# Optimization experiments

Measured on AMD Instinct MI355X. Metric: run time of the kernel, lower is better.

Reference implementation:

```python
import jax, jax.numpy as jnp
import numpy as np

EPS = 1e-5  # nn.LayerNorm default

def _ln(x, g, b):
    m = x.mean(-1, keepdims=True)
    v = ((x - m) ** 2).mean(-1, keepdims=True)
    return (x - m) / jnp.sqrt(v + EPS) * g + b


def setup_inputs() -> dict:
    key = jax.random.key(0)
    ks = jax.random.split(key, 16)
    B, T, H, W = 8, 20, 224, 224
    D, NC = 1536, 7
    s = 0.02
    f32 = jnp.float32
    return {
        'x': jax.random.normal(ks[0], (B, 3, T, H, W), f32),
        'timestamp': jax.random.uniform(ks[1], (B,), f32),
        # surrogate backbone: patchify conv (stride 16) + global avg pool -> 1536 feats
        'conv_w': jax.random.normal(ks[2], (D, 3, 16, 16), f32) * s,
        'conv_b': jnp.zeros((D,), f32),
        'w_red': jax.random.normal(ks[3], (D, D), f32) * s,
        'b_red': jnp.zeros((D,), f32),
        'w_num': jax.random.normal(ks[4], (D, 1), f32) * s,
        'b_num': jnp.zeros((D,), f32),
        'time_embed': jax.random.normal(ks[5], (1, T, D), f32) * s,
        'cls_swap': jax.random.normal(ks[6], (1, 5, 1, D), f32) * s,
        'ln_g': jnp.ones((D,), f32),
        'ln_b': jnp.zeros((D,), f32),
        'w_qkv': jax.random.normal(ks[7], (3 * D, D), f32) * s,
        'w_tproj': jax.random.normal(ks[8], (D, D), f32) * s,
        'b_tproj': jnp.zeros((D,), f32),
        'w_tfc': jax.random.normal(ks[9], (D, D), f32) * s,
        'b_tfc': jnp.zeros((D,), f32),
        'w_head': jax.random.normal(ks[10], (NC, D), f32) * s,
        'b_head': jnp.zeros((NC,), f32),
    }


def reference(x, timestamp, conv_w, conv_b, w_red, b_red, w_num, b_num,
              time_embed, cls_swap, ln_g, ln_b, w_qkv, w_tproj, b_tproj,
              w_tfc, b_tfc, w_head, b_head):
    B, C, T, H, W = x.shape
    D = w_red.shape[0]
    NH = 12
    HD = D // NH
    scale = HD ** -0.5

    # (b t) c h w  -> backbone surrogate -> (B*T, D)
    xf = jnp.transpose(x, (0, 2, 1, 3, 4)).reshape(B * T, C, H, W)
    f = jax.lax.conv_general_dilated(
        xf, conv_w, window_strides=(16, 16), padding='VALID',
        dimension_numbers=('NCHW', 'OIHW', 'NCHW'))
    f = (f + conv_b[None, :, None, None]).mean((2, 3))  # global avg pool -> (BT, D)

    xr = (f @ w_red.T + b_red).reshape(B, T, D)           # reduce_dim
    xt = xr + time_embed
    te = timestamp[:, None] @ w_num.T + b_num             # NumberToVector (B, D)
    xt = xt + te[:, None, :]

    # groups: b (n k) c -> b n k c, k=4, n=5; prepend 1 cls token per group
    g = jnp.concatenate(
        [jnp.broadcast_to(cls_swap, (B, 5, 1, D)), xt.reshape(B, 5, 4, D)], axis=2)

    for _ in range(4):  # num_interactions
        gr = g.reshape(B * 5, 5, D)
        hn = _ln(gr, ln_g, ln_b)
        qkv = (hn @ w_qkv.T).reshape(B * 5, 5, 3, NH, HD).transpose(2, 0, 3, 1, 4)
        q, k, v = qkv[0], qkv[1], qkv[2]                  # (b*n, h, t, hd)
        a = jax.nn.softmax(jnp.einsum('bhqd,bhkd->bhqk', q, k) * scale, axis=-1)
        o = jnp.einsum('bhqk,bhkd->bhqd', a, v).transpose(0, 2, 1, 3).reshape(B * 5, 5, D)
        o = o @ w_tproj.T + b_tproj                       # attn proj
        upd = (o @ w_tfc.T + b_tfc) + gr                  # temporal_fc + residual
        g = upd.reshape(B, 5, 5, D)
        # swap cls tokens between groups via roll
        g = g.at[:, :, 0, :].set(jnp.roll(g[:, :, 0, :], 1, axis=1))

    xt = g[:, :, 1:, :].reshape(B, T, D)
    out = xt[:, -1, :] + xr[:, -1, :]
    return out @ w_head.T + b_head  # (B, num_classes)
```

## Files before the change

kernel.cpp:

```cpp
#include <hip/hip_runtime.h>

typedef __attribute__((ext_vector_type(8))) short short8;
typedef __attribute__((ext_vector_type(8))) unsigned short ushort8;
typedef __attribute__((ext_vector_type(4))) float f32x4;
typedef unsigned short ushort_t;

__device__ __forceinline__ ushort_t f2bf(float f) {
    unsigned u = __builtin_bit_cast(unsigned, f);
    u += 0x7fffu + ((u >> 16) & 1u);
    return (ushort_t)(u >> 16);
}

__device__ __forceinline__ void load_lds16b(const void* gp, void* lp) {
    __builtin_amdgcn_global_load_lds(
        (const __attribute__((address_space(1))) void*)gp,
        (__attribute__((address_space(3))) void*)lp, 16, 0, 0);
}

__global__ __launch_bounds__(256, 2) void prep_kernel(
    const float* __restrict__ x, const float* __restrict__ w_qkv,
    const float* __restrict__ w_tf, const float* __restrict__ w_red,
    const float* __restrict__ conv_w, const float* __restrict__ w_tp,
    const float* __restrict__ b_tp, const float* __restrict__ b_tf,
    const float* __restrict__ conv_b, const float* __restrict__ b_red,
    const float* __restrict__ cls,
    ushort_t* __restrict__ AP, ushort_t* __restrict__ WQ,
    ushort_t* __restrict__ WF, ushort_t* __restrict__ WR,
    ushort_t* __restrict__ WCVT, ushort_t* __restrict__ WTT,
    float* __restrict__ BC, float* __restrict__ BC2,
    float* __restrict__ GA) {
    __shared__ __align__(16) float smem[64 * 68];
    int blk = blockIdx.x, tid = threadIdx.x;
    if (blk < 480) {
        int bt = blk / 3, c = blk % 3;
        int b = bt / 20, t = bt % 20;
        int w = tid >> 6, lane = tid & 63;
        int cl = lane < 56 ? lane : 55;
        const float* base = x + (size_t)((b * 3 + c) * 20 + t) * 50176
                              + (size_t)w * 224 + 4 * cl;
        f32x4 acc4[4];
        #pragma unroll
        for (int q = 0; q < 4; ++q) acc4[q] = (f32x4){0.f, 0.f, 0.f, 0.f};
        #pragma unroll
        for (int b16 = 0; b16 < 4; ++b16) {
            const int cnt = (b16 == 3) ? 8 : 16;
            f32x4 v[16];
            #pragma unroll
            for (int u = 0; u < 16; ++u) {
                if (u < cnt) {
                    int j = b16 * 16 + u;
                    v[u] = *(const f32x4*)(base + (size_t)j * 896);
                }
            }
            #pragma unroll
            for (int u = 0; u < 16; ++u)
                if (u < cnt) acc4[u & 3] += v[u];
        }
        if (lane >= 56) {
            #pragma unroll
            for (int q = 0; q < 4; ++q) acc4[q] = (f32x4){0.f, 0.f, 0.f, 0.f};
        }
        #pragma unroll
        for (int q = 0; q < 4; ++q) {
            #pragma unroll
            for (int m = 4; m <= 32; m <<= 1) {
                acc4[q][0] += __shfl_xor(acc4[q][0], m);
                acc4[q][1] += __shfl_xor(acc4[q][1], m);
                acc4[q][2] += __shfl_xor(acc4[q][2], m);
                acc4[q][3] += __shfl_xor(acc4[q][3], m);
            }
        }
        if (lane < 4) {
            #pragma unroll
            for (int q = 0; q < 4; ++q) {
                int i = w + 4 * q;
                ushort4 o;
                o.x = f2bf(acc4[q][0] * (1.f / 196.f));
                o.y = f2bf(acc4[q][1] * (1.f / 196.f));
                o.z = f2bf(acc4[q][2] * (1.f / 196.f));
                o.w = f2bf(acc4[q][3] * (1.f / 196.f));
                *(ushort4*)(AP + (size_t)bt * 768 + c * 256 + i * 16 + 4 * lane) = o;
            }
        }
    } else if (blk < 1920) {
        f32x4 va[4], vb[4];
        ushort_t* dst[4];
        long off[4];
        #pragma unroll
        for (int it = 0; it < 4; ++it) {
            long c = ((long)(blk - 480) * 4 + it) * 2048 + tid * 8;
            const float* s; ushort_t* d; long i;
            if (c < 7077888)       { s = w_qkv; d = WQ; i = c; }
            else if (c < 9437184)  { s = w_tf;  d = WF; i = c - 7077888; }
            else                   { s = w_red; d = WR; i = c - 9437184; }
            va[it] = *(const f32x4*)(s + i);
            vb[it] = *(const f32x4*)(s + i + 4);
            dst[it] = d; off[it] = i;
        }
        #pragma unroll
        for (int it = 0; it < 4; ++it) {
            ushort8 o;
            o[0] = f2bf(va[it][0]); o[1] = f2bf(va[it][1]);
            o[2] = f2bf(va[it][2]); o[3] = f2bf(va[it][3]);
            o[4] = f2bf(vb[it][0]); o[5] = f2bf(vb[it][1]);
            o[6] = f2bf(vb[it][2]); o[7] = f2bf(vb[it][3]);
            *(ushort8*)(dst[it] + off[it]) = o;
        }
    } else if (blk < 2496) {
        int tb = blk - 1920;
        int bi = tb / 24, bj = tb % 24;
        int r0 = (tid >> 4) << 2;
        int c0 = (tid & 15) << 2;
        #pragma unroll
        for (int rr = 0; rr < 4; ++rr) {
            f32x4 v = *(const f32x4*)(w_tp + (size_t)(bi * 64 + r0 + rr) * 1536 + bj * 64 + c0);
            smem[(r0 + rr) * 68 + c0 + 0] = v[0];
            smem[(r0 + rr) * 68 + c0 + 1] = v[1];
            smem[(r0 + rr) * 68 + c0 + 2] = v[2];
            smem[(r0 + rr) * 68 + c0 + 3] = v[3];
        }
        __syncthreads();
        #pragma unroll
        for (int rr = 0; rr < 4; ++rr) {
            int jj = r0 + rr;
            ushort4 o;
            o.x = f2bf(smem[(c0 + 0) * 68 + jj]);
            o.y = f2bf(smem[(c0 + 1) * 68 + jj]);
            o.z = f2bf(smem[(c0 + 2) * 68 + jj]);
            o.w = f2bf(smem[(c0 + 3) * 68 + jj]);
            *(ushort4*)(WTT + (size_t)(bj * 64 + jj) * 1536 + bi * 64 + c0) = o;
        }
    } else if (blk < 2784) {
        int tb = blk - 2496;
        int bi = tb / 12, bj = tb % 12;
        int r0 = (tid >> 4) << 2;
        int c0 = (tid & 15) << 2;
        #pragma unroll
        for (int rr = 0; rr < 4; ++rr) {
            f32x4 v = *(const f32x4*)(conv_w + (size_t)(bi * 64 + r0 + rr) * 768 + bj * 64 + c0);
            smem[(r0 + rr) * 68 + c0 + 0] = v[0];
            smem[(r0 + rr) * 68 + c0 + 1] = v[1];
            smem[(r0 + rr) * 68 + c0 + 2] = v[2];
            smem[(r0 + rr) * 68 + c0 + 3] = v[3];
        }
        __syncthreads();
        #pragma unroll
        for (int rr = 0; rr < 4; ++rr) {
            int jj = r0 + rr;
            ushort4 o;
            o.x = f2bf(smem[(c0 + 0) * 68 + jj]);
            o.y = f2bf(smem[(c0 + 1) * 68 + jj]);
            o.z = f2bf(smem[(c0 + 2) * 68 + jj]);
            o.w = f2bf(smem[(c0 + 3) * 68 + jj]);
            *(ushort4*)(WCVT + (size_t)(bj * 64 + jj) * 1536 + bi * 64 + c0) = o;
        }
    } else if (blk < 2824) {
        int cblk = blk - 2784;
        int b = cblk / 5, n = cblk % 5;
        size_t row = (size_t)(b * 25 + n * 5) * 1536;
        #pragma unroll
        for (int j = 0; j < 6; ++j) {
            int d = tid + j * 256;
            GA[row + d] = cls[n * 1536 + d];
        }
    } else if (blk < 2920) {
        int bb = blk - 2824;
        int row = bb * 16 + (tid >> 4);
        int sub = tid & 15;
        float acc = 0.f;
        for (int j = 0; j < 96; ++j) {
            int k = sub + j * 16;
            acc += w_tf[(size_t)row * 1536 + k] * b_tp[k];
        }
        acc += __shfl_xor(acc, 1); acc += __shfl_xor(acc, 2);
        acc += __shfl_xor(acc, 4); acc += __shfl_xor(acc, 8);
        if (sub == 0) BC[row] = acc + b_tf[row];
    } else {
        int bb = blk - 2920;
        int row = bb * 16 + (tid >> 4);
        int sub = tid & 15;
        float acc = 0.f;
        for (int j = 0; j < 48; ++j) {
            int n0 = sub + j * 16;
            acc += w_red[(size_t)row * 1536 + n0] * conv_b[n0];
            acc += w_red[(size_t)row * 1536 + n0 + 768] * conv_b[n0 + 768];
        }
        acc += __shfl_xor(acc, 1); acc += __shfl_xor(acc, 2);
        acc += __shfl_xor(acc, 4); acc += __shfl_xor(acc, 8);
        if (sub == 0) BC2[row] = acc + b_red[row];
    }
}

template <bool OUT_BF16>
__device__ __forceinline__ void gemm128_tile(
    char* lds, const ushort_t* __restrict__ A, const ushort_t* __restrict__ B,
    void* __restrict__ Cv, int M, int N, int K, int KS, int tn, int tm) {
    const int tid = threadIdx.x;
    const int lane = tid & 63;
    const int w = tid >> 6;
    const int wr = w >> 1, wc = w & 1;

    f32x4 acc[4][4];
    #pragma unroll
    for (int m = 0; m < 4; ++m)
        #pragma unroll
        for (int n = 0; n < 4; ++n)
            acc[m][n] = (f32x4){0.f, 0.f, 0.f, 0.f};

    const int nK = K >> 6;
    const int rbase = lane >> 3, cc = lane & 7;

    auto stage = [&](int k0, int buf) {
        char* lA = lds + buf * 32768;
        char* lB = lA + 16384;
        #pragma unroll
        for (int j = 0; j < 4; ++j) {
            int row = w * 32 + j * 8 + rbase;
            int cf = cc ^ (row & 7);
            int ga = tm * 128 + row; if (ga > M - 1) ga = M - 1;
            load_lds16b(A + (size_t)ga * KS + (k0 + cf * 8),
                        lA + (w * 32 + j * 8) * 128);
        }
        #pragma unroll
        for (int j = 0; j < 4; ++j) {
            int row = w * 32 + j * 8 + rbase;
            int cf = cc ^ (row & 7);
            load_lds16b(B + (size_t)(tn * 128 + row) * KS + (k0 + cf * 8),
                        lB + (w * 32 + j * 8) * 128);
        }
    };

    stage(0, 0);
    asm volatile("s_waitcnt vmcnt(0)" ::: "memory");
    __builtin_amdgcn_s_barrier();
    __builtin_amdgcn_sched_barrier(0);
    for (int t = 0; t < nK; ++t) {
        int cur = t & 1;
        if (t + 1 < nK) stage((t + 1) << 6, cur ^ 1);
        __builtin_amdgcn_sched_barrier(0);
        const char* lA = lds + cur * 32768;
        const char* lB = lA + 16384;
        #pragma unroll
        for (int ks = 0; ks < 2; ++ks) {
            short8 av[4], bv[4];
            const int rlo = lane & 15;
            const int chi = ks * 4 + (lane >> 4);
            #pragma unroll
            for (int m = 0; m < 4; ++m) {
                int r = wr * 64 + m * 16 + rlo;
                av[m] = *(const short8*)(lA + r * 128 + ((chi ^ (r & 7)) << 4));
            }
            #pragma unroll
            for (int n = 0; n < 4; ++n) {
                int r = wc * 64 + n * 16 + rlo;
                bv[n] = *(const short8*)(lB + r * 128 + ((chi ^ (r & 7)) << 4));
            }
            #pragma unroll
            for (int m = 0; m < 4; ++m)
                #pragma unroll
                for (int n = 0; n < 4; ++n)
                    acc[m][n] = __builtin_amdgcn_mfma_f32_16x16x32_bf16(
                        av[m], bv[n], acc[m][n], 0, 0, 0);
        }
        asm volatile("s_waitcnt vmcnt(0)" ::: "memory");
        __builtin_amdgcn_s_barrier();
        __builtin_amdgcn_sched_barrier(0);
    }

    const int c_l = lane & 15, r_q = (lane >> 4) * 4;
    #pragma unroll
    for (int m = 0; m < 4; ++m) {
        #pragma unroll
        for (int reg = 0; reg < 4; ++reg) {
            int r_ = tm * 128 + wr * 64 + m * 16 + r_q + reg;
            if (r_ < M) {
                #pragma unroll
                for (int n = 0; n < 4; ++n) {
                    int cc_ = tn * 128 + wc * 64 + n * 16 + c_l;
                    float v = acc[m][n][reg];
                    if (OUT_BF16) ((ushort_t*)Cv)[(size_t)r_ * N + cc_] = f2bf(v);
                    else          ((float*)Cv)[(size_t)r_ * N + cc_] = v;
                }
            }
        }
    }
}

__global__ __launch_bounds__(256) void wcf_kernel(
    const ushort_t* __restrict__ WF, const ushort_t* __restrict__ WTT,
    const ushort_t* __restrict__ WR, const ushort_t* __restrict__ WCVT,
    ushort_t* __restrict__ WC, ushort_t* __restrict__ WRC) {
    __shared__ __align__(16) char lds[65536];
    int task = blockIdx.x;
    if (task < 144)
        gemm128_tile<true>(lds, WF, WTT, WC, 1536, 1536, 1536, 1536,
                           task % 12, task / 12);
    else {
        int t2 = task - 144;
        gemm128_tile<true>(lds, WR, WCVT, WRC, 1536, 768, 1536, 1536,
                           t2 % 6, t2 / 6);
    }
}

template <int MT, bool OUT_BF16, bool HAS_BIAS, bool HAS_RES, bool CLS_SWAP, bool BUILD_G>
__device__ __forceinline__ void gemm_tile(
    char* lds, int lane, int tn, int tm,
    const ushort_t* __restrict__ A, const ushort_t* __restrict__ B,
    void* __restrict__ Cv, const float* __restrict__ bias,
    const float* __restrict__ res, int M, int N, int K, int KS,
    float* __restrict__ g_out, const float* __restrict__ temb,
    const float* __restrict__ ts, const float* __restrict__ w_num,
    const float* __restrict__ b_num) {
    constexpr int BUFB = MT * 2048 + 8192;

    f32x4 acc[MT][4];
    #pragma unroll
    for (int m = 0; m < MT; ++m)
        #pragma unroll
        for (int n = 0; n < 4; ++n)
            acc[m][n] = (f32x4){0.f, 0.f, 0.f, 0.f};

    const int nK = K >> 6;
    const int rbase = lane >> 3, cc = lane & 7;

    auto stage = [&](int k0, int buf) {
        char* lA = lds + buf * BUFB;
        char* lB = lA + MT * 2048;
        #pragma unroll
        for (int j = 0; j < MT * 2; ++j) {
            int row = j * 8 + rbase;
            int cf = cc ^ (row & 7);
            int ga = tm * (MT * 16) + row; if (ga > M - 1) ga = M - 1;
            load_lds16b(A + (size_t)ga * KS + (k0 + cf * 8), lA + j * 1024);
        }
        #pragma unroll
        for (int j = 0; j < 8; ++j) {
            int row = j * 8 + rbase;
            int cf = cc ^ (row & 7);
            load_lds16b(B + (size_t)(tn * 64 + row) * KS + (k0 + cf * 8), lB + j * 1024);
        }
    };

    stage(0, 0);
    for (int t = 0; t < nK; ++t) {
        int cur = t & 1;
        if (t + 1 < nK) {
            stage((t + 1) << 6, cur ^ 1);
            if constexpr (MT == 2) asm volatile("s_waitcnt vmcnt(12)" ::: "memory");
            else                   asm volatile("s_waitcnt vmcnt(16)" ::: "memory");
        } else {
            asm volatile("s_waitcnt vmcnt(0)" ::: "memory");
        }
        __builtin_amdgcn_sched_barrier(0);
        const char* lA = lds + cur * BUFB;
        const char* lB = lA + MT * 2048;
        #pragma unroll
        for (int ks = 0; ks < 2; ++ks) {
            short8 av[MT], bv[4];
            const int rlo = lane & 15;
            const int chi = ks * 4 + (lane >> 4);
            #pragma unroll
            for (int m = 0; m < MT; ++m) {
                int r = m * 16 + rlo;
                av[m] = *(const short8*)(lA + r * 128 + ((chi ^ (r & 7)) << 4));
            }
            #pragma unroll
            for (int n = 0; n < 4; ++n) {
                int r = n * 16 + rlo;
                bv[n] = *(const short8*)(lB + r * 128 + ((chi ^ (r & 7)) << 4));
            }
            #pragma unroll
            for (int m = 0; m < MT; ++m)
                #pragma unroll
                for (int n = 0; n < 4; ++n)
                    acc[m][n] = __builtin_amdgcn_mfma_f32_16x16x32_bf16(
                        av[m], bv[n], acc[m][n], 0, 0, 0);
        }
    }

    const int c_l = lane & 15, r_q = (lane >> 4) * 4;
    #pragma unroll
    for (int m = 0; m < MT; ++m) {
        #pragma unroll
        for (int reg = 0; reg < 4; ++reg) {
            int r_ = tm * (MT * 16) + m * 16 + r_q + reg;
            if (r_ < M) {
                int r2 = r_;
                if (CLS_SWAP) {
                    int bb = r_ / 25, rem = r_ % 25;
                    if (rem % 5 == 0) r2 = bb * 25 + ((rem / 5 + 1) % 5) * 5;
                }
                #pragma unroll
                for (int n = 0; n < 4; ++n) {
                    int cc_ = tn * 64 + n * 16 + c_l;
                    float v = acc[m][n][reg];
                    if (HAS_BIAS) v += bias[cc_];
                    if (HAS_RES) v += res[(size_t)r_ * N + cc_];
                    if (OUT_BF16) ((ushort_t*)Cv)[(size_t)r2 * N + cc_] = f2bf(v);
                    else          ((float*)Cv)[(size_t)r2 * N + cc_] = v;
                    if (BUILD_G) {
                        int b = r_ / 20, t = r_ % 20;
                        float gval = v + temb[t * 1536 + cc_] +
                                     ts[b] * w_num[cc_] + b_num[cc_];
                        g_out[(size_t)(b * 25 + (t / 4) * 5 + (t % 4) + 1) * 1536 + cc_] = gval;
                    }
                }
            }
        }
    }
}

__global__ __launch_bounds__(64) void xr_kernel(
    const ushort_t* __restrict__ AP, const ushort_t* __restrict__ WRC,
    float* __restrict__ XR, const float* __restrict__ BC2,
    float* __restrict__ GA, const float* __restrict__ temb,
    const float* __restrict__ ts, const float* __restrict__ w_num,
    const float* __restrict__ b_num) {
    __shared__ __align__(16) char lds[24576];
    gemm_tile<2, false, true, false, false, true>(
        lds, threadIdx.x, blockIdx.x, blockIdx.y, AP, WRC, XR, BC2, nullptr,
        160, 1536, 768, 768, GA, temb, ts, w_num, b_num);
}

__global__ __launch_bounds__(64) void qkv_kernel(
    const ushort_t* __restrict__ HN, const ushort_t* __restrict__ WQ,
    float* __restrict__ C0, float* __restrict__ C1) {
    __shared__ __align__(16) char lds[32768];
    int tn = blockIdx.x, tmh = blockIdx.y;
    int half = tmh >> 2, tm = tmh & 3;
    gemm_tile<4, false, false, false, false, false>(
        lds, threadIdx.x, tn, tm, HN + half * 768, WQ + half * 768,
        half ? C1 : C0, nullptr, nullptr, 200, 4608, 768, 1536,
        nullptr, nullptr, nullptr, nullptr, nullptr);
}

__global__ __launch_bounds__(64) void proj_kernel(
    const ushort_t* __restrict__ OBF, const ushort_t* __restrict__ WC,
    float* __restrict__ gdst, const float* __restrict__ BC,
    const float* __restrict__ gsrc) {
    __shared__ __align__(16) char lds[24576];
    gemm_tile<2, false, true, true, true, false>(
        lds, threadIdx.x, blockIdx.x, blockIdx.y, OBF, WC, gdst, BC, gsrc,
        200, 1536, 1536, 1536, nullptr, nullptr, nullptr, nullptr, nullptr);
}

__global__ __launch_bounds__(256) void ln_kernel(
    const float* __restrict__ g, const float* __restrict__ gamma,
    const float* __restrict__ beta, ushort_t* __restrict__ hn) {
    int r = blockIdx.x, tid = threadIdx.x;
    const float* x = g + (size_t)r * 1536;
    float v[6], s = 0.f, s2 = 0.f;
    #pragma unroll
    for (int j = 0; j < 6; ++j) {
        v[j] = x[tid + j * 256];
        s += v[j]; s2 += v[j] * v[j];
    }
    #pragma unroll
    for (int m = 1; m < 64; m <<= 1) { s += __shfl_xor(s, m); s2 += __shfl_xor(s2, m); }
    __shared__ float red[8];
    int wid = tid >> 6;
    if ((tid & 63) == 0) { red[wid] = s; red[4 + wid] = s2; }
    __syncthreads();
    s  = red[0] + red[1] + red[2] + red[3];
    s2 = red[4] + red[5] + red[6] + red[7];
    float mean = s * (1.0f / 1536.0f);
    float var  = s2 * (1.0f / 1536.0f) - mean * mean;
    float rstd = rsqrtf(var + 1e-5f);
    #pragma unroll
    for (int j = 0; j < 6; ++j) {
        int d = tid + j * 256;
        float y = (v[j] - mean) * rstd * gamma[d] + beta[d];
        hn[(size_t)r * 1536 + d] = f2bf(y);
    }
}

__global__ __launch_bounds__(64) void attn_kernel(
    const float* __restrict__ qA, const float* __restrict__ qB,
    ushort_t* __restrict__ o) {
    int gid = blockIdx.x;
    int h = gid % 12, gg = gid / 12;
    int l = threadIdx.x;
    size_t off = (size_t)gg * 5 * 4608 + h * 128 + 2 * l;
    const float* b0 = qA + off;
    const float* b1 = qB + off;
    float q[5][2], k[5][2], v[5][2];
    #pragma unroll
    for (int tt = 0; tt < 5; ++tt) {
        float2 q0 = *(const float2*)(b0 + tt * 4608);
        float2 q1 = *(const float2*)(b1 + tt * 4608);
        float2 k0 = *(const float2*)(b0 + tt * 4608 + 1536);
        float2 k1 = *(const float2*)(b1 + tt * 4608 + 1536);
        float2 v0 = *(const float2*)(b0 + tt * 4608 + 3072);
        float2 v1 = *(const float2*)(b1 + tt * 4608 + 3072);
        q[tt][0] = q0.x + q1.x; q[tt][1] = q0.y + q1.y;
        k[tt][0] = k0.x + k1.x; k[tt][1] = k0.y + k1.y;
        v[tt][0] = v0.x + v1.x; v[tt][1] = v0.y + v1.y;
    }
    float sc[5][5];
    #pragma unroll
    for (int i = 0; i < 5; ++i)
        #pragma unroll
        for (int j = 0; j < 5; ++j)
            sc[i][j] = q[i][0] * k[j][0] + q[i][1] * k[j][1];
    #pragma unroll
    for (int m = 1; m < 64; m <<= 1)
        #pragma unroll
        for (int i = 0; i < 5; ++i)
            #pragma unroll
            for (int j = 0; j < 5; ++j)
                sc[i][j] += __shfl_xor(sc[i][j], m);
    const float scale = 0.08838834764831845f;
    float a_[5][5];
    #pragma unroll
    for (int i = 0; i < 5; ++i) {
        float mx = -1e30f;
        #pragma unroll
        for (int j = 0; j < 5; ++j) mx = fmaxf(mx, sc[i][j]);
        float sum = 0.f;
        #pragma unroll
        for (int j = 0; j < 5; ++j) { a_[i][j] = __expf((sc[i][j] - mx) * scale); sum += a_[i][j]; }
        float inv = 1.0f / sum;
        #pragma unroll
        for (int j = 0; j < 5; ++j) a_[i][j] *= inv;
    }
    #pragma unroll
    for (int i = 0; i < 5; ++i) {
        float o0 = 0.f, o1 = 0.f;
        #pragma unroll
        for (int j = 0; j < 5; ++j) { o0 += a_[i][j] * v[j][0]; o1 += a_[i][j] * v[j][1]; }
        ushort2 w; w.x = f2bf(o0); w.y = f2bf(o1);
        *(ushort2*)(o + (size_t)(gg * 5 + i) * 1536 + h * 128 + 2 * l) = w;
    }
}

__global__ __launch_bounds__(64) void head_kernel(
    const float* __restrict__ gfin, const float* __restrict__ xr,
    const float* __restrict__ w_head, const float* __restrict__ b_head,
    float* __restrict__ out) {
    int b = blockIdx.x, l = threadIdx.x;
    const float* gv = gfin + (size_t)(b * 25 + 24) * 1536;
    const float* xv = xr + (size_t)(b * 20 + 19) * 1536;
    float acc[7] = {0, 0, 0, 0, 0, 0, 0};
    for (int d = l; d < 1536; d += 64) {
        float xval = gv[d] + xv[d];
        #pragma unroll
        for (int c = 0; c < 7; ++c) acc[c] += xval * w_head[c * 1536 + d];
    }
    #pragma unroll
    for (int c = 0; c < 7; ++c)
        #pragma unroll
        for (int m = 1; m < 64; m <<= 1) acc[c] += __shfl_xor(acc[c], m);
    if (l == 0) {
        #pragma unroll
        for (int c = 0; c < 7; ++c) out[b * 7 + c] = acc[c] + b_head[c];
    }
}

#define OFF_WQ    0u
#define OFF_WF    14155776u
#define OFF_WR    18874368u
#define OFF_WCVT  23592960u
#define OFF_WTT   25952256u
#define OFF_WC    30670848u
#define OFF_WRC   35389440u
#define OFF_BC    37748736u
#define OFF_BC2   37754880u
#define OFF_AP    37761024u
#define OFF_XR    38006784u
#define OFF_GA    38989824u
#define OFF_GB    40218624u
#define OFF_HN    41447424u
#define OFF_QKV0  42061824u
#define OFF_QKV1  45748224u
#define OFF_OBF   49434624u

extern "C" void kernel_launch(void* const* d_in, const int* in_sizes, int n_in,
                              void* d_out, int out_size, void* d_ws, size_t ws_size,
                              hipStream_t stream) {
    const float* x      = (const float*)d_in[0];
    const float* ts     = (const float*)d_in[1];
    const float* conv_w = (const float*)d_in[2];
    const float* conv_b = (const float*)d_in[3];
    const float* w_red  = (const float*)d_in[4];
    const float* b_red  = (const float*)d_in[5];
    const float* w_num  = (const float*)d_in[6];
    const float* b_num  = (const float*)d_in[7];
    const float* temb   = (const float*)d_in[8];
    const float* cls    = (const float*)d_in[9];
    const float* ln_g   = (const float*)d_in[10];
    const float* ln_b   = (const float*)d_in[11];
    const float* w_qkv  = (const float*)d_in[12];
    const float* w_tp   = (const float*)d_in[13];
    const float* b_tp   = (const float*)d_in[14];
    const float* w_tf   = (const float*)d_in[15];
    const float* b_tf   = (const float*)d_in[16];
    const float* w_head = (const float*)d_in[17];
    const float* b_head = (const float*)d_in[18];

    char* ws = (char*)d_ws;
    ushort_t* WQ   = (ushort_t*)(ws + OFF_WQ);
    ushort_t* WF   = (ushort_t*)(ws + OFF_WF);
    ushort_t* WR   = (ushort_t*)(ws + OFF_WR);
    ushort_t* WCVT = (ushort_t*)(ws + OFF_WCVT);
    ushort_t* WTT  = (ushort_t*)(ws + OFF_WTT);
    ushort_t* WC   = (ushort_t*)(ws + OFF_WC);
    ushort_t* WRC  = (ushort_t*)(ws + OFF_WRC);
    float*    BC   = (float*)(ws + OFF_BC);
    float*    BC2  = (float*)(ws + OFF_BC2);
    ushort_t* AP   = (ushort_t*)(ws + OFF_AP);
    float*    XR   = (float*)(ws + OFF_XR);
    float*    GA   = (float*)(ws + OFF_GA);
    float*    GB   = (float*)(ws + OFF_GB);
    ushort_t* HN   = (ushort_t*)(ws + OFF_HN);
    float*    QKV0 = (float*)(ws + OFF_QKV0);
    float*    QKV1 = (float*)(ws + OFF_QKV1);
    ushort_t* OBF  = (ushort_t*)(ws + OFF_OBF);

    prep_kernel<<<3016, 256, 0, stream>>>(x, w_qkv, w_tf, w_red, conv_w, w_tp,
                                          b_tp, b_tf, conv_b, b_red, cls,
                                          AP, WQ, WF, WR, WCVT, WTT, BC, BC2, GA);
    wcf_kernel<<<216, 256, 0, stream>>>(WF, WTT, WR, WCVT, WC, WRC);
    xr_kernel<<<dim3(24, 5), 64, 0, stream>>>(AP, WRC, XR, BC2, GA,
                                              temb, ts, w_num, b_num);
    float* gsrc = GA;
    float* gdst = GB;
    for (int it = 0; it < 4; ++it) {
        ln_kernel<<<200, 256, 0, stream>>>(gsrc, ln_g, ln_b, HN);
        qkv_kernel<<<dim3(72, 8), 64, 0, stream>>>(HN, WQ, QKV0, QKV1);
        attn_kernel<<<480, 64, 0, stream>>>(QKV0, QKV1, OBF);
        proj_kernel<<<dim3(24, 7), 64, 0, stream>>>(OBF, WC, gdst, BC, gsrc);
        float* tmp = gsrc; gsrc = gdst; gdst = tmp;
    }
    head_kernel<<<8, 64, 0, stream>>>(gsrc, XR, w_head, b_head, (float*)d_out);
}
```

Baseline: 199.6 us.

## Stage pooling and weight-cast loads through LDS with async global_load_lds

The patch-pool branch now streams image rows into a double-buffered LDS staging area with direct global-to-LDS loads, then reduces from LDS per output element instead of using register accumulators and shuffles. The weight-to-bf16 cast branch likewise loads each chunk into LDS asynchronously and converts from there. The aim is deeper memory-level parallelism on these bandwidth-bound prep stages. The cost is a much larger shared-memory footprint (about 65 KB), which can cut occupancy, plus extra barriers.

```diff
diff --git a/kernel.cpp b/kernel.cpp
--- a/kernel.cpp
+++ b/kernel.cpp
@@ -29,82 +29,73 @@
     ushort_t* __restrict__ WCVT, ushort_t* __restrict__ WTT,
     float* __restrict__ BC, float* __restrict__ BC2,
     float* __restrict__ GA) {
-    __shared__ __align__(16) float smem[64 * 68];
+    __shared__ __align__(16) char ldsb[66560];
+    float* smem = (float*)ldsb;
     int blk = blockIdx.x, tid = threadIdx.x;
     if (blk < 480) {
         int bt = blk / 3, c = blk % 3;
         int b = bt / 20, t = bt % 20;
+        const char* img = (const char*)(x + (size_t)((b * 3 + c) * 20 + t) * 50176);
         int w = tid >> 6, lane = tid & 63;
-        int cl = lane < 56 ? lane : 55;
-        const float* base = x + (size_t)((b * 3 + c) * 20 + t) * 50176
-                              + (size_t)w * 224 + 4 * cl;
-        f32x4 acc4[4];
-        #pragma unroll
-        for (int q = 0; q < 4; ++q) acc4[q] = (f32x4){0.f, 0.f, 0.f, 0.f};
-        #pragma unroll
-        for (int b16 = 0; b16 < 4; ++b16) {
-            const int cnt = (b16 == 3) ? 8 : 16;
-            f32x4 v[16];
-            #pragma unroll
-            for (int u = 0; u < 16; ++u) {
-                if (u < cnt) {
-                    int j = b16 * 16 + u;
-                    v[u] = *(const f32x4*)(base + (size_t)j * 896);
-                }
-            }
-            #pragma unroll
-            for (int u = 0; u < 16; ++u)
-                if (u < cnt) acc4[u & 3] += v[u];
-        }
-        if (lane >= 56) {
-            #pragma unroll
-            for (int q = 0; q < 4; ++q) acc4[q] = (f32x4){0.f, 0.f, 0.f, 0.f};
-        }
-        #pragma unroll
-        for (int q = 0; q < 4; ++q) {
-            #pragma unroll
-            for (int m = 4; m <= 32; m <<= 1) {
-                acc4[q][0] += __shfl_xor(acc4[q][0], m);
-                acc4[q][1] += __shfl_xor(acc4[q][1], m);
-                acc4[q][2] += __shfl_xor(acc4[q][2], m);
-                acc4[q][3] += __shfl_xor(acc4[q][3], m);
-            }
-        }
-        if (lane < 4) {
-            #pragma unroll
-            for (int q = 0; q < 4; ++q) {
-                int i = w + 4 * q;
-                ushort4 o;
-                o.x = f2bf(acc4[q][0] * (1.f / 196.f));
-                o.y = f2bf(acc4[q][1] * (1.f / 196.f));
-                o.z = f2bf(acc4[q][2] * (1.f / 196.f));
-                o.w = f2bf(acc4[q][3] * (1.f / 196.f));
-                *(ushort4*)(AP + (size_t)bt * 768 + c * 256 + i * 16 + 4 * lane) = o;
-            }
-        }
+        int laneoff = lane < 56 ? lane * 16 : 0;
+        auto stagep = [&](int k, int buf) {
+            #pragma unroll
+            for (int j2 = 0; j2 < 8; ++j2) {
+                int rl = w * 8 + j2;
+                int grow = k * 32 + rl;
+                load_lds16b(img + (size_t)grow * 896 + laneoff,
+                            ldsb + buf * 33280 + rl * 1040);
+            }
+        };
+        int i = tid >> 4, j = tid & 15;
+        float acc = 0.f;
+        const float* lf = (const float*)ldsb;
+        stagep(0, 0);
+        for (int k = 0; k < 7; ++k) {
+            if (k + 1 < 7) {
+                stagep(k + 1, (k + 1) & 1);
+                asm volatile("s_waitcnt vmcnt(8)" ::: "memory");
+            } else {
+                asm volatile("s_waitcnt vmcnt(0)" ::: "memory");
+            }
+            __builtin_amdgcn_s_barrier();
+            __builtin_amdgcn_sched_barrier(0);
+            int bb = (k & 1) * 8320;
+            #pragma unroll
+            for (int rr = 0; rr < 2; ++rr) {
+                int rl = i + rr * 16;
+                #pragma unroll
+                for (int q = 0; q < 14; ++q)
+                    acc += lf[bb + rl * 260 + q * 16 + j];
+            }
+            __builtin_amdgcn_s_barrier();
+            __builtin_amdgcn_sched_barrier(0);
+        }
+        AP[(size_t)bt * 768 + c * 256 + i * 16 + j] = f2bf(acc * (1.f / 196.f));
     } else if (blk < 1920) {
-        f32x4 va[4], vb[4];
-        ushort_t* dst[4];
-        long off[4];
-        #pragma unroll
-        for (int it = 0; it < 4; ++it) {
-            long c = ((long)(blk - 480) * 4 + it) * 2048 + tid * 8;
-            const float* s; ushort_t* d; long i;
-            if (c < 7077888)       { s = w_qkv; d = WQ; i = c; }
-            else if (c < 9437184)  { s = w_tf;  d = WF; i = c - 7077888; }
-            else                   { s = w_red; d = WR; i = c - 9437184; }
-            va[it] = *(const f32x4*)(s + i);
-            vb[it] = *(const f32x4*)(s + i + 4);
-            dst[it] = d; off[it] = i;
-        }
-        #pragma unroll
-        for (int it = 0; it < 4; ++it) {
-            ushort8 o;
-            o[0] = f2bf(va[it][0]); o[1] = f2bf(va[it][1]);
-            o[2] = f2bf(va[it][2]); o[3] = f2bf(va[it][3]);
-            o[4] = f2bf(vb[it][0]); o[5] = f2bf(vb[it][1]);
-            o[6] = f2bf(vb[it][2]); o[7] = f2bf(vb[it][3]);
-            *(ushort8*)(dst[it] + off[it]) = o;
+        int blk2 = blk - 480;
+        long base = (long)blk2 * 8192;
+        const float* s; ushort_t* d; long i0;
+        if (blk2 < 864)       { s = w_qkv; d = WQ; i0 = base; }
+        else if (blk2 < 1152) { s = w_tf;  d = WF; i0 = base - 7077888; }
+        else                  { s = w_red; d = WR; i0 = base - 9437184; }
+        int w = tid >> 6, lane = tid & 63;
+        #pragma unroll
+        for (int j2 = 0; j2 < 8; ++j2) {
+            int slot = w * 8 + j2;
+            load_lds16b((const char*)(s + i0 + slot * 256) + lane * 16,
+                        ldsb + slot * 1024);
+        }
+        asm volatile("s_waitcnt vmcnt(0)" ::: "memory");
+        __builtin_amdgcn_s_barrier();
+        __builtin_amdgcn_sched_barrier(0);
+        const f32x4* lf4 = (const f32x4*)ldsb;
+        #pragma unroll
+        for (int r = 0; r < 8; ++r) {
+            f32x4 v = lf4[r * 256 + tid];
+            ushort4 o;
+            o.x = f2bf(v[0]); o.y = f2bf(v[1]); o.z = f2bf(v[2]); o.w = f2bf(v[3]);
+            *(ushort4*)(d + i0 + r * 1024 + tid * 4) = o;
         }
     } else if (blk < 2496) {
         int tb = blk - 1920;
```

Result: no change. 199.0 us (-0.3%).
